# Kernel optimization log

Hardware: AMD Instinct MI355X
Metric: run time of the kernel (lower is better)

The kernel has to match this reference:

```python
import jax, jax.numpy as jnp
import numpy as np

B, H, W, C = 4, 256, 256, 32
K = 5  # per-pixel kernel spatial size (K*K = 25 taps)


def setup_inputs() -> dict:
    key = jax.random.key(0)
    k1, k2, k3 = jax.random.split(key, 3)
    feat = jax.random.normal(k1, (B, H, W, C), dtype=jnp.float32)
    kernel = jax.random.normal(k2, (B, H, W, K * K), dtype=jnp.float32)
    bias = jax.random.normal(k3, (C,), dtype=jnp.float32)
    return {"feat": feat, "kernel": kernel, "bias": bias}


def reference(feat, kernel, bias):
    # Per-pixel predicted convolution (kernel prediction network style):
    # out[b,h,w,c] = sum_{i,j} feat[b, h+i-p, w+j-p, c] * kernel[b,h,w, i*K+j]
    # Kernel taps are shared across channels; SAME zero padding.
    b, h, w, c = feat.shape
    kk = kernel.shape[-1]
    k = int(round(np.sqrt(kk)))
    pad = k // 2
    fp = jnp.pad(feat, ((0, 0), (pad, pad), (pad, pad), (0, 0)))
    out = jnp.zeros_like(feat)
    for i in range(k):          # small fixed K*K loop; avoids materializing
        for j in range(k):      # the [B,H,W,K*K,C] patch tensor
            tap = kernel[..., i * k + j][..., None]          # [B,H,W,1]
            out = out + fp[:, i:i + h, j:j + w, :] * tap      # [B,H,W,C]
    return out + bias  # tf.nn.bias_add, channels_last
```

## Files before the change

kernel.cpp:

```cpp
#include <hip/hip_runtime.h>


#define BB 4
#define HH 256
#define WW 256
#define CC 32
#define KK 5
#define VH 8
#define TW 32
#define TPB 256
#define TROWS (VH + KK - 1)
#define TCOLS (TW + KK - 1)
#define SF_F4 (TROWS * TCOLS * CC / 4)
#define SK_F4 (VH * TW * KK * KK / 4)
#define NQF (SF_F4 / 64)
#define NQ  ((SF_F4 + SK_F4) / 64)

typedef __attribute__((address_space(1))) const void gvoid_t;
typedef __attribute__((address_space(3))) void svoid_t;

__global__ __launch_bounds__(TPB, 2) void kpn_conv_kernel(
    const float* __restrict__ feat,
    const float* __restrict__ kern,
    const float* __restrict__ bias,
    float* __restrict__ out)
{
    __shared__ float4 sb[SF_F4 + SK_F4];

    const int t    = threadIdx.x;
    const int lane = t & 63;
    const int wave = t >> 6;

    const int bw = blockIdx.x & 7;
    const int bh = (blockIdx.x >> 3) & 31;
    const int b  = blockIdx.x >> 8;
    const int h0 = bh * VH;
    const int w0 = bw * TW;

    const float* fb = feat + (((size_t)b) << 16) * CC;
    const float* kb = kern + (size_t)((b * HH + h0) * WW + w0) * (KK * KK);

    for (int q = wave; q < NQ; q += TPB / 64) {
        if (q < NQF) {
            int e   = (q << 6) + lane;
            int row = e / (TCOLS * CC / 4);
            int rem = e - row * (TCOLS * CC / 4);
            int col = rem >> 3;
            int c4  = rem & 7;
            int hc  = min(max(h0 + row - (KK / 2), 0), HH - 1);
            int wc  = min(max(w0 + col - (KK / 2), 0), WW - 1);
            const float* gp = fb + ((((size_t)hc << 8) + wc) << 5) + (c4 << 2);
            __builtin_amdgcn_global_load_lds((gvoid_t*)gp,
                                             (svoid_t*)(sb + (q << 6)),
                                             16, 0, 0);
        } else {
            int e   = ((q - NQF) << 6) + lane;
            int oh  = e / 200;
            int off = (e - oh * 200) << 2;
            const float* gp = kb + (size_t)oh * (WW * KK * KK) + off;
            __builtin_amdgcn_global_load_lds((gvoid_t*)gp,
                                             (svoid_t*)(sb + SF_F4 + ((q - NQF) << 6)),
                                             16, 0, 0);
        }
    }
    __syncthreads();

    const bool wlo = (w0 == 0), whi = (w0 == WW - TW);
    if (h0 == 0 || h0 == HH - VH || wlo || whi) {
        const float4 z = make_float4(0.f, 0.f, 0.f, 0.f);
        #pragma unroll
        for (int r = 0; r < TROWS; ++r) {
            int hraw = h0 + r - (KK / 2);
            if (hraw < 0 || hraw >= HH) {
                for (int s = t; s < TCOLS * CC / 4; s += TPB)
                    sb[r * (TCOLS * CC / 4) + s] = z;
            }
        }
        if (wlo && t < 192) {
            int r = t >> 4, c = (t >> 3) & 1, c4 = t & 7;
            sb[r * (TCOLS * CC / 4) + c * 8 + c4] = z;
        }
        if (whi && t < 192) {
            int r = t >> 4, c = (TCOLS - 2) + ((t >> 3) & 1), c4 = t & 7;
            sb[r * (TCOLS * CC / 4) + c * 8 + c4] = z;
        }
        __syncthreads();
    }

    const int cg = (t & 7) << 2;
    const int wL = t >> 3;
    const float* sf  = (const float*)sb;
    const float* skw = (const float*)(sb + SF_F4);

    const float4 bz = *(const float4*)(bias + cg);
    float4 acc[VH];
    #pragma unroll
    for (int oh = 0; oh < VH; ++oh) acc[oh] = bz;

    #pragma unroll
    for (int r = 0; r < TROWS; ++r) {
        float4 f[KK];
        #pragma unroll
        for (int j = 0; j < KK; ++j)
            f[j] = *(const float4*)(sf + (r * TCOLS + wL + j) * CC + cg);

        #pragma unroll
        for (int oh = 0; oh < VH; ++oh) {
            const int i = r - oh;
            if (i >= 0 && i < KK) {
                const float* wp = skw + (oh * TW + wL) * (KK * KK) + i * KK;
                const float wg0 = wp[0], wg1 = wp[1], wg2 = wp[2],
                            wg3 = wp[3], wg4 = wp[4];
                acc[oh].x += f[0].x*wg0 + f[1].x*wg1 + f[2].x*wg2 + f[3].x*wg3 + f[4].x*wg4;
                acc[oh].y += f[0].y*wg0 + f[1].y*wg1 + f[2].y*wg2 + f[3].y*wg3 + f[4].y*wg4;
                acc[oh].z += f[0].z*wg0 + f[1].z*wg1 + f[2].z*wg2 + f[3].z*wg3 + f[4].z*wg4;
                acc[oh].w += f[0].w*wg0 + f[1].w*wg1 + f[2].w*wg2 + f[3].w*wg3 + f[4].w*wg4;
            }
        }
    }

    #pragma unroll
    for (int oh = 0; oh < VH; ++oh) {
        const size_t pix = (size_t)(b * HH + h0 + oh) * WW + (w0 + wL);
        *(float4*)(out + pix * CC + cg) = acc[oh];
    }
}

extern "C" void kernel_launch(void* const* d_in, const int* in_sizes, int n_in,
                              void* d_out, int out_size, void* d_ws, size_t ws_size,
                              hipStream_t stream) {
    const float* feat = (const float*)d_in[0];
    const float* kern = (const float*)d_in[1];
    const float* bias = (const float*)d_in[2];
    float* out = (float*)d_out;

    dim3 grid(BB * (HH / VH) * (WW / TW));
    dim3 block(TPB);
    kpn_conv_kernel<<<grid, block, 0, stream>>>(feat, kern, bias, out);
}
```

Baseline: 106.5 us.

## Split tile loads into two phases and overlap second half with compute

Reorders the async global-to-LDS loads so the first half of the kernel weights and feature rows (enough for output rows 0-3) are issued first. Interior blocks then wait only on partial vmcnt counts before computing the first four output rows, and wait for the rest before computing the second four. Edge blocks keep the full sync plus zero-fill path. This is meant to hide part of the load latency behind compute, at the cost of hand-tuned vmcnt counts that must match the per-wave issue order exactly.

Result: slower. 109.4 us (+2.7%).

```diff
diff --git a/kernel.cpp b/kernel.cpp
--- a/kernel.cpp
+++ b/kernel.cpp
@@ -13,8 +13,8 @@
 #define TCOLS (TW + KK - 1)
 #define SF_F4 (TROWS * TCOLS * CC / 4)
 #define SK_F4 (VH * TW * KK * KK / 4)
-#define NQF (SF_F4 / 64)
 #define NQ  ((SF_F4 + SK_F4) / 64)
+#define NQ1 49
 
 typedef __attribute__((address_space(1))) const void gvoid_t;
 typedef __attribute__((address_space(3))) void svoid_t;
@@ -40,9 +40,19 @@
     const float* fb = feat + (((size_t)b) << 16) * CC;
     const float* kb = kern + (size_t)((b * HH + h0) * WW + w0) * (KK * KK);
 
-    for (int q = wave; q < NQ; q += TPB / 64) {
-        if (q < NQF) {
-            int e   = (q << 6) + lane;
+    auto issue = [&](int q) {
+        if (q < 13 || (q >= NQ1 && q < 61)) {
+            int kq  = (q < 13) ? q : q - 36;
+            int e   = (kq << 6) + lane;
+            int oh  = e / 200;
+            int off = (e - oh * 200) << 2;
+            const float* gp = kb + (size_t)oh * (WW * KK * KK) + off;
+            __builtin_amdgcn_global_load_lds((gvoid_t*)gp,
+                                             (svoid_t*)(sb + SF_F4 + (kq << 6)),
+                                             16, 0, 0);
+        } else {
+            int fq  = (q < NQ1) ? q - 13 : q - 25;
+            int e   = (fq << 6) + lane;
             int row = e / (TCOLS * CC / 4);
             int rem = e - row * (TCOLS * CC / 4);
             int col = rem >> 3;
@@ -51,22 +61,64 @@
             int wc  = min(max(w0 + col - (KK / 2), 0), WW - 1);
             const float* gp = fb + ((((size_t)hc << 8) + wc) << 5) + (c4 << 2);
             __builtin_amdgcn_global_load_lds((gvoid_t*)gp,
-                                             (svoid_t*)(sb + (q << 6)),
-                                             16, 0, 0);
-        } else {
-            int e   = ((q - NQF) << 6) + lane;
-            int oh  = e / 200;
-            int off = (e - oh * 200) << 2;
-            const float* gp = kb + (size_t)oh * (WW * KK * KK) + off;
-            __builtin_amdgcn_global_load_lds((gvoid_t*)gp,
-                                             (svoid_t*)(sb + SF_F4 + ((q - NQF) << 6)),
+                                             (svoid_t*)(sb + (fq << 6)),
                                              16, 0, 0);
         }
+    };
+    for (int q = wave; q < NQ1; q += TPB / 64) issue(q);
+    for (int q = NQ1 + wave; q < NQ; q += TPB / 64) issue(q);
+
+    const int cg = (t & 7) << 2;
+    const int wL = t >> 3;
+    const float* sf  = (const float*)sb;
+    const float* skw = (const float*)(sb + SF_F4);
+
+    const float4 bz = *(const float4*)(bias + cg);
+    float4 acc[VH];
+    #pragma unroll
+    for (int oh = 0; oh < VH; ++oh) acc[oh] = bz;
+
+#define COMPUTE_PHASE(OHB)                                                    \
+    {                                                                         \
+        _Pragma("unroll")                                                     \
+        for (int r8 = 0; r8 < 8; ++r8) {                                      \
+            const int r = (OHB) + r8;                                         \
+            float4 f[KK];                                                     \
+            _Pragma("unroll")                                                 \
+            for (int j = 0; j < KK; ++j)                                      \
+                f[j] = *(const float4*)(sf + (r * TCOLS + wL + j) * CC + cg); \
+            _Pragma("unroll")                                                 \
+            for (int o4 = 0; o4 < 4; ++o4) {                                  \
+                const int i = r8 - o4;                                        \
+                if (i >= 0 && i < KK) {                                       \
+                    const int oh = (OHB) + o4;                                \
+                    const float* wp = skw + (oh * TW + wL) * (KK * KK) + i * KK; \
+                    const float wg0 = wp[0], wg1 = wp[1], wg2 = wp[2],        \
+                                wg3 = wp[3], wg4 = wp[4];                     \
+                    acc[oh].x += f[0].x*wg0 + f[1].x*wg1 + f[2].x*wg2 + f[3].x*wg3 + f[4].x*wg4; \
+                    acc[oh].y += f[0].y*wg0 + f[1].y*wg1 + f[2].y*wg2 + f[3].y*wg3 + f[4].y*wg4; \
+                    acc[oh].z += f[0].z*wg0 + f[1].z*wg1 + f[2].z*wg2 + f[3].z*wg3 + f[4].z*wg4; \
+                    acc[oh].w += f[0].w*wg0 + f[1].w*wg1 + f[2].w*wg2 + f[3].w*wg3 + f[4].w*wg4; \
+                }                                                             \
+            }                                                                 \
+        }                                                                     \
     }
-    __syncthreads();
 
     const bool wlo = (w0 == 0), whi = (w0 == WW - TW);
-    if (h0 == 0 || h0 == HH - VH || wlo || whi) {
+    const bool edge = (h0 == 0) || (h0 == HH - VH) || wlo || whi;
+
+    if (!edge) {
+        if (wave < 2) asm volatile("s_waitcnt vmcnt(8)" ::: "memory");
+        else          asm volatile("s_waitcnt vmcnt(7)" ::: "memory");
+        __builtin_amdgcn_s_barrier();
+        __builtin_amdgcn_sched_barrier(0);
+        COMPUTE_PHASE(0);
+        asm volatile("s_waitcnt vmcnt(0)" ::: "memory");
+        __builtin_amdgcn_s_barrier();
+        __builtin_amdgcn_sched_barrier(0);
+        COMPUTE_PHASE(4);
+    } else {
+        __syncthreads();
         const float4 z = make_float4(0.f, 0.f, 0.f, 0.f);
         #pragma unroll
         for (int r = 0; r < TROWS; ++r) {
@@ -85,38 +137,8 @@
             sb[r * (TCOLS * CC / 4) + c * 8 + c4] = z;
         }
         __syncthreads();
-    }
-
-    const int cg = (t & 7) << 2;
-    const int wL = t >> 3;
-    const float* sf  = (const float*)sb;
-    const float* skw = (const float*)(sb + SF_F4);
-
-    const float4 bz = *(const float4*)(bias + cg);
-    float4 acc[VH];
-    #pragma unroll
-    for (int oh = 0; oh < VH; ++oh) acc[oh] = bz;
-
-    #pragma unroll
-    for (int r = 0; r < TROWS; ++r) {
-        float4 f[KK];
-        #pragma unroll
-        for (int j = 0; j < KK; ++j)
-            f[j] = *(const float4*)(sf + (r * TCOLS + wL + j) * CC + cg);
-
-        #pragma unroll
-        for (int oh = 0; oh < VH; ++oh) {
-            const int i = r - oh;
-            if (i >= 0 && i < KK) {
-                const float* wp = skw + (oh * TW + wL) * (KK * KK) + i * KK;
-                const float wg0 = wp[0], wg1 = wp[1], wg2 = wp[2],
-                            wg3 = wp[3], wg4 = wp[4];
-                acc[oh].x += f[0].x*wg0 + f[1].x*wg1 + f[2].x*wg2 + f[3].x*wg3 + f[4].x*wg4;
-                acc[oh].y += f[0].y*wg0 + f[1].y*wg1 + f[2].y*wg2 + f[3].y*wg3 + f[4].y*wg4;
-                acc[oh].z += f[0].z*wg0 + f[1].z*wg1 + f[2].z*wg2 + f[3].z*wg3 + f[4].z*wg4;
-                acc[oh].w += f[0].w*wg0 + f[1].w*wg1 + f[2].w*wg2 + f[3].w*wg3 + f[4].w*wg4;
-            }
-        }
+        COMPUTE_PHASE(0);
+        COMPUTE_PHASE(4);
     }
 
     #pragma unroll
```
